# Optimization experiments

Hardware: AMD Instinct MI355X
Metric: run time of the kernel (lower is better)

Reference implementation:

```python
import jax, jax.numpy as jnp
import numpy as np

VOCAB = 32000
NUM_CLASS = 16
HID = 256
BATCH = 2048  # c dim
NSTEP = 1     # n dim


def setup_inputs() -> dict:
    key = jax.random.key(0)
    ks = jax.random.split(key, 8)
    x = jax.random.randint(ks[0], (BATCH,), 0, VOCAB)
    z = jax.random.randint(ks[1], (NSTEP, BATCH), 0, NUM_CLASS)
    h = jax.random.normal(ks[2], (BATCH, NSTEP, HID), dtype=jnp.float32)
    E = jax.random.normal(ks[3], (VOCAB, HID), dtype=jnp.float32) * 0.02
    Vw = jax.random.normal(ks[4], (VOCAB, HID), dtype=jnp.float32) * 0.02
    Vb = jnp.zeros((VOCAB,), dtype=jnp.float32)
    W = jax.random.normal(ks[5], (NUM_CLASS, HID, HID), dtype=jnp.float32) * 0.02
    U = jax.random.normal(ks[6], (NUM_CLASS, HID, HID), dtype=jnp.float32) * 0.02
    return {"x": x, "z": z, "h": h, "E": E, "Vw": Vw, "Vb": Vb, "W": W, "U": U}


def reference(x, z, h, E, Vw, Vb, W, U):
    # e: (c, hid) embedding lookup
    e = E[x]
    # gather per-class weight banks: (n, c, k, h)
    Wz = W[z]
    Uz = U[z]
    # batched GEMV over gathered weights + tanh RNN step -> (n, c, k)
    h_t = jnp.tanh(
        jnp.einsum('nckh,ch->nck', Wz, e)
        + jnp.einsum('nckh,cnh->nck', Uz, h)
    ).transpose(1, 0, 2)  # (c, n, k)
    # output projection V: (c, n, vocab)
    logits = jnp.einsum('cnk,vk->cnv', h_t, Vw) + Vb
    return (logits, h_t)
```

## Files before the change

kernel.cpp:

```cpp
#include <hip/hip_runtime.h>
#include <hip/hip_bf16.h>

#define VOCAB 32000
#define NUM_CLASS 16
#define HID 256
#define KCAT 512
#define BATCH 2048

typedef __attribute__((ext_vector_type(8))) __bf16 bf16x8;
typedef __attribute__((ext_vector_type(4))) float floatx4;

__device__ __forceinline__ unsigned short f32_to_bf16_u16(float f) {
    union { float f; unsigned u; } a;
    a.f = f;
    unsigned r = a.u + 0x7fffu + ((a.u >> 16) & 1u);
    return (unsigned short)(r >> 16);
}

struct bf8v { unsigned short s[8]; };

__global__ __launch_bounds__(256) void bucket_kernel(
    const int* __restrict__ z, int* __restrict__ perm,
    int* __restrict__ counts, int* __restrict__ bases)
{
    __shared__ int s_cnt[NUM_CLASS];
    __shared__ int s_off[NUM_CLASS];
    const int t = threadIdx.x;
    if (t < NUM_CLASS) s_cnt[t] = 0;
    __syncthreads();
    for (int c = t; c < BATCH; c += 256) atomicAdd(&s_cnt[z[c]], 1);
    __syncthreads();
    if (t == 0) {
        int acc = 0;
        for (int i = 0; i < NUM_CLASS; ++i) { s_off[i] = acc; acc += s_cnt[i]; }
    }
    __syncthreads();
    if (t < NUM_CLASS) { counts[t] = s_cnt[t]; bases[t] = s_off[t]; }
    __syncthreads();
    for (int c = t; c < BATCH; c += 256) {
        int p = atomicAdd(&s_off[z[c]], 1);
        perm[p] = c;
    }
}

__global__ __launch_bounds__(256) void gather_g_kernel(
    const int* __restrict__ x, const float* __restrict__ E,
    const float* __restrict__ h, unsigned short* __restrict__ G)
{
    const int tid = blockIdx.x * 256 + threadIdx.x;
    const int c  = tid >> 6;
    const int j0 = (tid & 63) * 8;
    const float* src = (j0 < HID)
        ? (E + (size_t)x[c] * HID + j0)
        : (h + (size_t)c * HID + (j0 - HID));
    float4 v0 = ((const float4*)src)[0];
    float4 v1 = ((const float4*)src)[1];
    bf8v o;
    o.s[0] = f32_to_bf16_u16(v0.x); o.s[1] = f32_to_bf16_u16(v0.y);
    o.s[2] = f32_to_bf16_u16(v0.z); o.s[3] = f32_to_bf16_u16(v0.w);
    o.s[4] = f32_to_bf16_u16(v1.x); o.s[5] = f32_to_bf16_u16(v1.y);
    o.s[6] = f32_to_bf16_u16(v1.z); o.s[7] = f32_to_bf16_u16(v1.w);
    *(bf8v*)(G + (size_t)c * KCAT + j0) = o;
}

__global__ __launch_bounds__(256) void cast_wu_kernel(
    const float* __restrict__ W, const float* __restrict__ U,
    unsigned short* __restrict__ Bcat)
{
    const int tid = blockIdx.x * 256 + threadIdx.x;
    const int row = tid >> 6;
    const int j0  = (tid & 63) * 8;
    const float* src = (j0 < HID)
        ? (W + (size_t)row * HID + j0)
        : (U + (size_t)row * HID + (j0 - HID));
    float4 v0 = ((const float4*)src)[0];
    float4 v1 = ((const float4*)src)[1];
    bf8v o;
    o.s[0] = f32_to_bf16_u16(v0.x); o.s[1] = f32_to_bf16_u16(v0.y);
    o.s[2] = f32_to_bf16_u16(v0.z); o.s[3] = f32_to_bf16_u16(v0.w);
    o.s[4] = f32_to_bf16_u16(v1.x); o.s[5] = f32_to_bf16_u16(v1.y);
    o.s[6] = f32_to_bf16_u16(v1.z); o.s[7] = f32_to_bf16_u16(v1.w);
    *(bf8v*)(Bcat + (size_t)row * KCAT + j0) = o;
}

struct bf4 { unsigned short s[4]; };

__global__ __launch_bounds__(256) void cvt_vw_kernel(
    const float* __restrict__ src, unsigned short* __restrict__ dst, int n4)
{
    int i = blockIdx.x * blockDim.x + threadIdx.x;
    const int stride = gridDim.x * blockDim.x;
    for (; i < n4; i += stride) {
        float4 v = ((const float4*)src)[i];
        bf4 o;
        o.s[0] = f32_to_bf16_u16(v.x);
        o.s[1] = f32_to_bf16_u16(v.y);
        o.s[2] = f32_to_bf16_u16(v.z);
        o.s[3] = f32_to_bf16_u16(v.w);
        ((bf4*)dst)[i] = o;
    }
}

__global__ __launch_bounds__(256) void rnn_gemm_kernel(
    const unsigned short* __restrict__ G,
    const unsigned short* __restrict__ Bcat,
    const int* __restrict__ perm, const int* __restrict__ counts,
    const int* __restrict__ bases,
    float* __restrict__ ht_f32, unsigned short* __restrict__ ht_bf16)
{
    const int g = blockIdx.y;
    const int cnt = counts[g];
    const int mstart = blockIdx.x * 32;
    if (mstart >= cnt) return;
    const int base = bases[g];

    __shared__ int s_rows[32];
    if (threadIdx.x < 32) {
        int mi = mstart + threadIdx.x;
        s_rows[threadIdx.x] = perm[base + (mi < cnt ? mi : cnt - 1)];
    }
    __syncthreads();

    const int lane = threadIdx.x & 63;
    const int wave = threadIdx.x >> 6;
    const int n0   = wave * 64;
    const int lrow = lane & 15;
    const int quad = lane >> 4;
    const int kq   = quad * 8;

    const unsigned short* Bg = Bcat + (size_t)g * HID * KCAT;

    floatx4 acc[2][4] = {};
#pragma unroll 4
    for (int k0 = 0; k0 < KCAT; k0 += 32) {
        bf16x8 a[2], b[4];
#pragma unroll
        for (int mi = 0; mi < 2; ++mi) {
            const int row = s_rows[mi * 16 + lrow];
            a[mi] = *(const bf16x8*)(G + (size_t)row * KCAT + k0 + kq);
        }
#pragma unroll
        for (int ni = 0; ni < 4; ++ni)
            b[ni] = *(const bf16x8*)(Bg + (size_t)(n0 + ni * 16 + lrow) * KCAT + k0 + kq);
#pragma unroll
        for (int mi = 0; mi < 2; ++mi)
#pragma unroll
            for (int ni = 0; ni < 4; ++ni)
                acc[mi][ni] = __builtin_amdgcn_mfma_f32_16x16x32_bf16(
                    a[mi], b[ni], acc[mi][ni], 0, 0, 0);
    }

#pragma unroll
    for (int mi = 0; mi < 2; ++mi) {
#pragma unroll
        for (int r = 0; r < 4; ++r) {
            const int midx = mi * 16 + quad * 4 + r;
            if (mstart + midx >= cnt) continue;
            const int c = s_rows[midx];
#pragma unroll
            for (int ni = 0; ni < 4; ++ni) {
                const int k = n0 + ni * 16 + lrow;
                const float v = tanhf(acc[mi][ni][r]);
                ht_f32 [(size_t)c * HID + k] = v;
                ht_bf16[(size_t)c * HID + k] = f32_to_bf16_u16(v);
            }
        }
    }
}

__global__ __launch_bounds__(256) void out_gemm_kernel(
    const unsigned short* __restrict__ A,
    const unsigned short* __restrict__ B,
    const float* __restrict__ Vb,
    float* __restrict__ C)
{
    const int lane = threadIdx.x & 63;
    const int wave = threadIdx.x >> 6;
    const int wr = wave >> 1, wc = wave & 1;
    const int m_wave = blockIdx.y * 128 + wr * 64;
    const int n_wave = blockIdx.x * 128 + wc * 64;
    const int lrow = lane & 15;
    const int quad = lane >> 4;
    const int kq   = quad * 8;

    floatx4 acc[4][4] = {};

#pragma unroll
    for (int k0 = 0; k0 < HID; k0 += 32) {
        bf16x8 a[4], b[4];
#pragma unroll
        for (int mi = 0; mi < 4; ++mi)
            a[mi] = *(const bf16x8*)(A + (size_t)(m_wave + mi * 16 + lrow) * HID + k0 + kq);
#pragma unroll
        for (int ni = 0; ni < 4; ++ni)
            b[ni] = *(const bf16x8*)(B + (size_t)(n_wave + ni * 16 + lrow) * HID + k0 + kq);
#pragma unroll
        for (int mi = 0; mi < 4; ++mi)
#pragma unroll
            for (int ni = 0; ni < 4; ++ni)
                acc[mi][ni] = __builtin_amdgcn_mfma_f32_16x16x32_bf16(
                    a[mi], b[ni], acc[mi][ni], 0, 0, 0);
    }

    const int row_q = quad * 4;
#pragma unroll
    for (int ni = 0; ni < 4; ++ni) {
        const int col = n_wave + ni * 16 + lrow;
        const float vb = Vb[col];
#pragma unroll
        for (int mi = 0; mi < 4; ++mi) {
            const int row = m_wave + mi * 16 + row_q;
            float* cp = C + (size_t)row * VOCAB + col;
#pragma unroll
            for (int r = 0; r < 4; ++r)
                cp[(size_t)r * VOCAB] = acc[mi][ni][r] + vb;
        }
    }
}

extern "C" void kernel_launch(void* const* d_in, const int* in_sizes, int n_in,
                              void* d_out, int out_size, void* d_ws, size_t ws_size,
                              hipStream_t stream) {
    const int*   x  = (const int*)d_in[0];
    const int*   z  = (const int*)d_in[1];
    const float* h  = (const float*)d_in[2];
    const float* E  = (const float*)d_in[3];
    const float* Vw = (const float*)d_in[4];
    const float* Vb = (const float*)d_in[5];
    const float* W  = (const float*)d_in[6];
    const float* U  = (const float*)d_in[7];

    float* logits = (float*)d_out;
    float* ht_out = logits + (size_t)BATCH * VOCAB;

    char* p = (char*)d_ws;
    unsigned short* Vw_bf = (unsigned short*)p;  p += (size_t)VOCAB * HID * 2;
    unsigned short* ht_bf = (unsigned short*)p;  p += (size_t)BATCH * HID * 2;
    unsigned short* G     = (unsigned short*)p;  p += (size_t)BATCH * KCAT * 2;
    unsigned short* Bcat  = (unsigned short*)p;  p += (size_t)NUM_CLASS * HID * KCAT * 2;
    int* perm   = (int*)p;  p += BATCH * 4;
    int* counts = (int*)p;  p += NUM_CLASS * 4;
    int* bases  = (int*)p;  p += NUM_CLASS * 4;

    bucket_kernel<<<1, 256, 0, stream>>>(z, perm, counts, bases);
    gather_g_kernel<<<BATCH * KCAT / 8 / 256, 256, 0, stream>>>(x, E, h, G);
    cast_wu_kernel<<<NUM_CLASS * HID * KCAT / 8 / 256, 256, 0, stream>>>(W, U, Bcat);
    cvt_vw_kernel<<<2048, 256, 0, stream>>>(Vw, Vw_bf, VOCAB * HID / 4);
    rnn_gemm_kernel<<<dim3(BATCH / 32, NUM_CLASS), 256, 0, stream>>>(
        G, Bcat, perm, counts, bases, ht_out, ht_bf);
    out_gemm_kernel<<<dim3(VOCAB / 128, BATCH / 128), 256, 0, stream>>>(ht_bf, Vw_bf, Vb, logits);
}
```

Baseline: 478.1 us.

## Stage output GEMM tiles in swizzled LDS, remap blocks, fuse prep kernels

The three conversion kernels become one prep kernel, which saves two launches. The output GEMM now stages 128x64 tiles of A and B into LDS through direct global-to-LDS loads with an XOR swizzle, so operands are read from shared memory instead of straight from global memory. It also remaps block IDs to group work across 8 XCD-like slices and writes logits with nontemporal stores. The cost is extra syncthreads with no double buffering, and the block remap assumes exactly 4000 blocks.

Measured after the change: 419.2 us. 1.14x faster.

```diff
diff --git a/kernel.cpp b/kernel.cpp
--- a/kernel.cpp
+++ b/kernel.cpp
@@ -19,6 +19,12 @@
 
 struct bf8v { unsigned short s[8]; };
 
+__device__ __forceinline__ void lds_load16(unsigned short* lds, const unsigned short* g) {
+    __builtin_amdgcn_global_load_lds(
+        (const __attribute__((address_space(1))) unsigned int*)g,
+        (__attribute__((address_space(3))) unsigned int*)lds, 16, 0, 0);
+}
+
 __global__ __launch_bounds__(256) void bucket_kernel(
     const int* __restrict__ z, int* __restrict__ perm,
     int* __restrict__ counts, int* __restrict__ bases)
@@ -43,16 +49,40 @@
     }
 }
 
-__global__ __launch_bounds__(256) void gather_g_kernel(
+#define PREP_G   (BATCH * KCAT / 8)
+#define PREP_WU  (NUM_CLASS * HID * KCAT / 8)
+#define PREP_VW  (VOCAB * HID / 8)
+#define PREP_TOT (PREP_G + PREP_WU + PREP_VW)
+
+__global__ __launch_bounds__(256) void prep_kernel(
     const int* __restrict__ x, const float* __restrict__ E,
-    const float* __restrict__ h, unsigned short* __restrict__ G)
+    const float* __restrict__ h,
+    const float* __restrict__ W, const float* __restrict__ U,
+    const float* __restrict__ Vw,
+    unsigned short* __restrict__ G, unsigned short* __restrict__ Bcat,
+    unsigned short* __restrict__ Vw_bf)
 {
     const int tid = blockIdx.x * 256 + threadIdx.x;
-    const int c  = tid >> 6;
-    const int j0 = (tid & 63) * 8;
-    const float* src = (j0 < HID)
-        ? (E + (size_t)x[c] * HID + j0)
-        : (h + (size_t)c * HID + (j0 - HID));
+    const float* src;
+    unsigned short* dst;
+    if (tid < PREP_G) {
+        const int c  = tid >> 6;
+        const int j0 = (tid & 63) * 8;
+        src = (j0 < HID) ? (E + (size_t)x[c] * HID + j0)
+                         : (h + (size_t)c * HID + (j0 - HID));
+        dst = G + (size_t)c * KCAT + j0;
+    } else if (tid < PREP_G + PREP_WU) {
+        const int idx = tid - PREP_G;
+        const int row = idx >> 6;
+        const int j0  = (idx & 63) * 8;
+        src = (j0 < HID) ? (W + (size_t)row * HID + j0)
+                         : (U + (size_t)row * HID + (j0 - HID));
+        dst = Bcat + (size_t)row * KCAT + j0;
+    } else {
+        const int idx = tid - (PREP_G + PREP_WU);
+        src = Vw + (size_t)idx * 8;
+        dst = Vw_bf + (size_t)idx * 8;
+    }
     float4 v0 = ((const float4*)src)[0];
     float4 v1 = ((const float4*)src)[1];
     bf8v o;
@@ -60,45 +90,7 @@
     o.s[2] = f32_to_bf16_u16(v0.z); o.s[3] = f32_to_bf16_u16(v0.w);
     o.s[4] = f32_to_bf16_u16(v1.x); o.s[5] = f32_to_bf16_u16(v1.y);
     o.s[6] = f32_to_bf16_u16(v1.z); o.s[7] = f32_to_bf16_u16(v1.w);
-    *(bf8v*)(G + (size_t)c * KCAT + j0) = o;
-}
-
-__global__ __launch_bounds__(256) void cast_wu_kernel(
-    const float* __restrict__ W, const float* __restrict__ U,
-    unsigned short* __restrict__ Bcat)
-{
-    const int tid = blockIdx.x * 256 + threadIdx.x;
-    const int row = tid >> 6;
-    const int j0  = (tid & 63) * 8;
-    const float* src = (j0 < HID)
-        ? (W + (size_t)row * HID + j0)
-        : (U + (size_t)row * HID + (j0 - HID));
-    float4 v0 = ((const float4*)src)[0];
-    float4 v1 = ((const float4*)src)[1];
-    bf8v o;
-    o.s[0] = f32_to_bf16_u16(v0.x); o.s[1] = f32_to_bf16_u16(v0.y);
-    o.s[2] = f32_to_bf16_u16(v0.z); o.s[3] = f32_to_bf16_u16(v0.w);
-    o.s[4] = f32_to_bf16_u16(v1.x); o.s[5] = f32_to_bf16_u16(v1.y);
-    o.s[6] = f32_to_bf16_u16(v1.z); o.s[7] = f32_to_bf16_u16(v1.w);
-    *(bf8v*)(Bcat + (size_t)row * KCAT + j0) = o;
-}
-
-struct bf4 { unsigned short s[4]; };
-
-__global__ __launch_bounds__(256) void cvt_vw_kernel(
-    const float* __restrict__ src, unsigned short* __restrict__ dst, int n4)
-{
-    int i = blockIdx.x * blockDim.x + threadIdx.x;
-    const int stride = gridDim.x * blockDim.x;
-    for (; i < n4; i += stride) {
-        float4 v = ((const float4*)src)[i];
-        bf4 o;
-        o.s[0] = f32_to_bf16_u16(v.x);
-        o.s[1] = f32_to_bf16_u16(v.y);
-        o.s[2] = f32_to_bf16_u16(v.z);
-        o.s[3] = f32_to_bf16_u16(v.w);
-        ((bf4*)dst)[i] = o;
-    }
+    *(bf8v*)dst = o;
 }
 
 __global__ __launch_bounds__(256) void rnn_gemm_kernel(
@@ -174,46 +166,75 @@
     const float* __restrict__ Vb,
     float* __restrict__ C)
 {
+    __shared__ unsigned short sA[128 * 64];
+    __shared__ unsigned short sB[128 * 64];
+
+    const int id  = blockIdx.x;
+    const int sid = (id & 7) * 500 + (id >> 3);
+    const int n0  = (sid >> 4) * 128;
+    const int m0  = (sid & 15) * 128;
+
     const int lane = threadIdx.x & 63;
     const int wave = threadIdx.x >> 6;
     const int wr = wave >> 1, wc = wave & 1;
-    const int m_wave = blockIdx.y * 128 + wr * 64;
-    const int n_wave = blockIdx.x * 128 + wc * 64;
     const int lrow = lane & 15;
     const int quad = lane >> 4;
-    const int kq   = quad * 8;
+
+    const int srow   = lane >> 3;
+    const int schunk = (lane & 7) ^ srow;
 
     floatx4 acc[4][4] = {};
 
 #pragma unroll
-    for (int k0 = 0; k0 < HID; k0 += 32) {
-        bf16x8 a[4], b[4];
-#pragma unroll
-        for (int mi = 0; mi < 4; ++mi)
-            a[mi] = *(const bf16x8*)(A + (size_t)(m_wave + mi * 16 + lrow) * HID + k0 + kq);
-#pragma unroll
-        for (int ni = 0; ni < 4; ++ni)
-            b[ni] = *(const bf16x8*)(B + (size_t)(n_wave + ni * 16 + lrow) * HID + k0 + kq);
-#pragma unroll
-        for (int mi = 0; mi < 4; ++mi)
-#pragma unroll
-            for (int ni = 0; ni < 4; ++ni)
-                acc[mi][ni] = __builtin_amdgcn_mfma_f32_16x16x32_bf16(
-                    a[mi], b[ni], acc[mi][ni], 0, 0, 0);
-    }
-
-    const int row_q = quad * 4;
+    for (int kt = 0; kt < 4; ++kt) {
+        const int k0 = kt * 64;
+        __syncthreads();
+#pragma unroll
+        for (int it = 0; it < 4; ++it) {
+            const int wl = wave * 4 + it;
+            const int r  = wl * 8 + srow;
+            lds_load16(&sA[wl * 512], A + (size_t)(m0 + r) * HID + k0 + schunk * 8);
+            lds_load16(&sB[wl * 512], B + (size_t)(n0 + r) * HID + k0 + schunk * 8);
+        }
+        __syncthreads();
+
+#pragma unroll
+        for (int ks = 0; ks < 2; ++ks) {
+            bf16x8 a[4], b[4];
+#pragma unroll
+            for (int mi = 0; mi < 4; ++mi) {
+                const int ra = wr * 64 + mi * 16 + lrow;
+                const int s  = (ks * 4 + quad) ^ (ra & 7);
+                a[mi] = *(const bf16x8*)&sA[ra * 64 + s * 8];
+            }
+#pragma unroll
+            for (int ni = 0; ni < 4; ++ni) {
+                const int rb = wc * 64 + ni * 16 + lrow;
+                const int s  = (ks * 4 + quad) ^ (rb & 7);
+                b[ni] = *(const bf16x8*)&sB[rb * 64 + s * 8];
+            }
+#pragma unroll
+            for (int mi = 0; mi < 4; ++mi)
+#pragma unroll
+                for (int ni = 0; ni < 4; ++ni)
+                    acc[mi][ni] = __builtin_amdgcn_mfma_f32_16x16x32_bf16(
+                        a[mi], b[ni], acc[mi][ni], 0, 0, 0);
+        }
+    }
+
+    const int m_wave = m0 + wr * 64;
+    const int n_wave = n0 + wc * 64;
+    const int row_q  = quad * 4;
 #pragma unroll
     for (int ni = 0; ni < 4; ++ni) {
         const int col = n_wave + ni * 16 + lrow;
         const float vb = Vb[col];
 #pragma unroll
         for (int mi = 0; mi < 4; ++mi) {
-            const int row = m_wave + mi * 16 + row_q;
-            float* cp = C + (size_t)row * VOCAB + col;
+            float* cp = C + (size_t)(m_wave + mi * 16 + row_q) * VOCAB + col;
 #pragma unroll
             for (int r = 0; r < 4; ++r)
-                cp[(size_t)r * VOCAB] = acc[mi][ni][r] + vb;
+                __builtin_nontemporal_store(acc[mi][ni][r] + vb, cp + (size_t)r * VOCAB);
         }
     }
 }
@@ -243,10 +264,8 @@
     int* bases  = (int*)p;  p += NUM_CLASS * 4;
 
     bucket_kernel<<<1, 256, 0, stream>>>(z, perm, counts, bases);
-    gather_g_kernel<<<BATCH * KCAT / 8 / 256, 256, 0, stream>>>(x, E, h, G);
-    cast_wu_kernel<<<NUM_CLASS * HID * KCAT / 8 / 256, 256, 0, stream>>>(W, U, Bcat);
-    cvt_vw_kernel<<<2048, 256, 0, stream>>>(Vw, Vw_bf, VOCAB * HID / 4);
+    prep_kernel<<<PREP_TOT / 256, 256, 0, stream>>>(x, E, h, W, U, Vw, G, Bcat, Vw_bf);
     rnn_gemm_kernel<<<dim3(BATCH / 32, NUM_CLASS), 256, 0, stream>>>(
         G, Bcat, perm, counts, bases, ht_out, ht_bf);
-    out_gemm_kernel<<<dim3(VOCAB / 128, BATCH / 128), 256, 0, stream>>>(ht_bf, Vw_bf, Vb, logits);
-}
+    out_gemm_kernel<<<4000, 256, 0, stream>>>(ht_bf, Vw_bf, Vb, logits);
+}
```
